# Optimization experiments

Hardware: AMD Instinct MI355X
Metric: run time of the kernel (lower is better)

The kernel has to match this reference:

```python
import jax, jax.numpy as jnp
import numpy as np

B, N, D, H = 64, 257, 1024, 16
HD = D // H  # 64


def setup_inputs() -> dict:
    key = jax.random.key(0)
    k1, k2, k3, k4, k5, k6 = jax.random.split(key, 6)
    x = jax.random.normal(k1, (B, N, D), dtype=jnp.float32)
    # boolean key mask per batch; never mask CLS token (col 0) so no fully-masked rows
    mask = jax.random.randint(k2, (B, N), 0, 2) > 0
    mask = mask.at[:, 0].set(False)
    s = 1.0 / np.sqrt(D)
    in_proj_w = jax.random.normal(k3, (3 * D, D), dtype=jnp.float32) * s
    in_proj_b = jax.random.normal(k4, (3 * D,), dtype=jnp.float32) * 0.02
    out_proj_w = jax.random.normal(k5, (D, D), dtype=jnp.float32) * s
    out_proj_b = jax.random.normal(k6, (D,), dtype=jnp.float32) * 0.02
    return {"x": x, "mask": mask, "in_proj_w": in_proj_w, "in_proj_b": in_proj_b,
            "out_proj_w": out_proj_w, "out_proj_b": out_proj_b}


def reference(x, mask, in_proj_w, in_proj_b, out_proj_w, out_proj_b):
    b, n, d = x.shape
    h, hd = H, d // H
    # fused QKV projection: [b, n, 3*d]
    qkv = jnp.einsum('bnd,ed->bne', x, in_proj_w) + in_proj_b
    # einops 'b n (qkv h d) -> qkv b h n d'
    qkv = qkv.reshape(b, n, 3, h, hd).transpose(2, 0, 3, 1, 4)
    q, k, v = qkv[0], qkv[1], qkv[2]  # each [b, h, n, hd]
    attn_weights = jnp.einsum('bhqe,bhke->bhqk', q, k) / jnp.sqrt(jnp.asarray(hd, x.dtype))
    # mode == 'mask': -inf on masked keys (broadcast over heads and queries)
    attn_weights = jnp.where(mask[:, None, None, :], -jnp.inf, attn_weights)
    attn_matrix = jax.nn.softmax(attn_weights, axis=-1)
    out = jnp.einsum('bhqk,bhke->bhqe', attn_matrix, v)  # [b, h, n, hd]
    out = out.transpose(0, 2, 1, 3).reshape(b, n, d)      # 'b h n d -> b n (h d)'
    return jnp.einsum('bnd,ed->bne', out, out_proj_w) + out_proj_b
```

## Files before the change

### kernel.cpp

```cpp
#include <hip/hip_runtime.h>

#define B_   64
#define N_   257
#define D_   1024
#define H_   16
#define HD_  64
#define M_   (B_*N_)
#define CK_  96
#define VTS_ 128
#define PLS_ 104

typedef __bf16 bf16x8 __attribute__((ext_vector_type(8)));
typedef __bf16 bf16x4 __attribute__((ext_vector_type(4)));
typedef float  f32x4  __attribute__((ext_vector_type(4)));

__device__ __forceinline__ void gload_lds16(const void* g, void* l) {
    __builtin_amdgcn_global_load_lds(
        (const __attribute__((address_space(1))) void*)g,
        (__attribute__((address_space(3))) void*)l, 16, 0, 0);
}

#define MEMF() asm volatile("" ::: "memory")
#define BARRIER() do { MEMF(); __builtin_amdgcn_s_barrier(); MEMF(); } while (0)
#define WAITV(n) asm volatile("s_waitcnt vmcnt(" #n ")" ::: "memory")

#define XQ_  4210688
#define W1Q_ 786432
#define W2Q_ 262144
__global__ __launch_bounds__(256) void cvt_all(const float* __restrict__ x,
                                               const float* __restrict__ w1,
                                               const float* __restrict__ w2,
                                               __bf16* __restrict__ xb,
                                               __bf16* __restrict__ w1b,
                                               __bf16* __restrict__ w2b) {
    int i = blockIdx.x * 256 + threadIdx.x;
    const float* src; __bf16* dst; int j;
    if (i < XQ_) { src = x; dst = xb; j = i; }
    else if (i < XQ_ + W1Q_) { src = w1; dst = w1b; j = i - XQ_; }
    else if (i < XQ_ + W1Q_ + W2Q_) { src = w2; dst = w2b; j = i - XQ_ - W1Q_; }
    else return;
    float4 v = reinterpret_cast<const float4*>(src)[j];
    bf16x4 o;
    o[0] = (__bf16)v.x; o[1] = (__bf16)v.y; o[2] = (__bf16)v.z; o[3] = (__bf16)v.w;
    *reinterpret_cast<bf16x4*>(dst + (size_t)j * 4) = o;
}

template<int NT, int MODE>
__global__ __launch_bounds__(512, 2) void gemm256(const __bf16* __restrict__ A,
                                                  const __bf16* __restrict__ W,
                                                  const float* __restrict__ bias,
                                                  __bf16* __restrict__ qo,
                                                  __bf16* __restrict__ ko,
                                                  __bf16* __restrict__ vo,
                                                  float* __restrict__ fo) {
    __shared__ __align__(16) char smem[131072];
    constexpr int NWG = 64 * NT;
    constexpr int qd = NWG >> 3;
    const int orig = blockIdx.x;
    const int xcd = orig & 7, loc = orig >> 3;
    const int wgid = xcd * qd + loc;
    const int rowt = wgid / NT, colt = wgid - rowt * NT;
    const int row0 = rowt * 256, col0 = colt * 256;

    const int tid = threadIdx.x, lane = tid & 63, wv = tid >> 6;
    const int wm = wv >> 2, wn = wv & 3;
    const int fr = lane & 15, fq = lane >> 4, frs = lane & 7;

    const int pr = tid >> 3;
    const int pg = ((tid & 7) ^ (pr & 7)) * 8;
    int srcA[4];
    {
        const int prow[4] = {0, 128, 64, 192};
#pragma unroll
        for (int p = 0; p < 4; ++p) {
            const int rg = row0 + prow[p] + pr;
            srcA[p] = rg * 1024 + pg;
        }
    }
    int srcW[2], ldsW[2];
#pragma unroll
    for (int e = 0; e < 2; ++e) {
        const int wb = (wv >> 1) * 64 + e * 16 + (wv & 1) * 8;
        srcW[e] = (col0 + wb + (lane >> 3)) * 1024 + pg;
        ldsW[e] = wb * 128;
    }
    char* const At0 = smem;
    char* const At1 = smem + 32768;
    char* const Wt0 = smem + 65536;
    char* const Wt1 = smem + 98304;

#define STG_AF(dst, kk) do { gload_lds16(A + srcA[0] + (kk), (dst) + wv * 1024); \
                             gload_lds16(A + srcA[1] + (kk), (dst) + 16384 + wv * 1024); } while (0)
#define STG_AB(dst, kk) do { gload_lds16(A + srcA[2] + (kk), (dst) + 8192 + wv * 1024); \
                             gload_lds16(A + srcA[3] + (kk), (dst) + 24576 + wv * 1024); } while (0)
#define STG_WF(dst, kk) do { gload_lds16(W + srcW[0] + (kk), (dst) + ldsW[0]); \
                             gload_lds16(W + srcW[1] + (kk), (dst) + ldsW[1]); } while (0)
#define STG_WB(dst, kk) do { gload_lds16(W + srcW[0] + 32768 + (kk), (dst) + ldsW[0] + 4096); \
                             gload_lds16(W + srcW[1] + 32768 + (kk), (dst) + ldsW[1] + 4096); } while (0)
#define LD_A(buf, rqo) do { \
    _Pragma("unroll") for (int i = 0; i < 4; ++i) \
    _Pragma("unroll") for (int ks = 0; ks < 2; ++ks) \
        af[i][ks] = *(const bf16x8*)((buf) + (wm * 128 + (rqo) + i * 16 + fr) * 128 \
                                           + (((ks * 4 + fq) ^ frs) << 4)); \
} while (0)
#define LD_B(buf, co, bw) do { \
    _Pragma("unroll") for (int j = 0; j < 2; ++j) \
    _Pragma("unroll") for (int ks = 0; ks < 2; ++ks) \
        bw[j][ks] = *(const bf16x8*)((buf) + (wn * 64 + (co) + j * 16 + fr) * 128 \
                                           + (((ks * 4 + fq) ^ frs) << 4)); \
} while (0)
#define MFMA_Q(i0, j0, bw) do { \
    __builtin_amdgcn_s_setprio(1); \
    _Pragma("unroll") for (int i = 0; i < 4; ++i) \
    _Pragma("unroll") for (int j = 0; j < 2; ++j) \
    _Pragma("unroll") for (int ks = 0; ks < 2; ++ks) \
        acc[(i0) + i][(j0) + j] = __builtin_amdgcn_mfma_f32_16x16x32_bf16( \
            af[i][ks], bw[j][ks], acc[(i0) + i][(j0) + j], 0, 0, 0); \
    __builtin_amdgcn_s_setprio(0); \
} while (0)

    f32x4 acc[8][4] = {};
    bf16x8 af[4][2], bw0[2][2], bw1[2][2];

    STG_AF(At0, 0); STG_WF(Wt0, 0); STG_WB(Wt0, 0); STG_AB(At0, 0);
    WAITV(0);
    BARRIER();

#pragma unroll 2
    for (int t = 0; t < 16; ++t) {
        char* const Ac = (t & 1) ? At1 : At0;
        char* const Wc = (t & 1) ? Wt1 : Wt0;
        char* const An = (t & 1) ? At0 : At1;
        char* const Wn = (t & 1) ? Wt0 : Wt1;
        if (t < 15) {
            const int kk = (t + 1) * 64;
            STG_AF(An, kk); STG_WF(Wn, kk); STG_WB(Wn, kk); STG_AB(An, kk);
        }
        LD_A(Ac, 0);
        LD_B(Wc, 0, bw0);
        LD_B(Wc, 32, bw1);
        MFMA_Q(0, 0, bw0);
        MFMA_Q(0, 2, bw1);
        LD_A(Ac, 64);
        MFMA_Q(4, 2, bw1);
        MFMA_Q(4, 0, bw0);
        WAITV(0);
        BARRIER();
    }

    if constexpr (MODE == 0) {
        const int which = colt >> 2;
        __bf16* const dst = which == 0 ? qo : (which == 1 ? ko : vo);
        const float scale = which == 0 ? 0.125f : 1.0f;
        float bj[4];
#pragma unroll
        for (int j = 0; j < 4; ++j) bj[j] = bias[col0 + wn * 64 + j * 16 + fr];
        __bf16* const Ct = (__bf16*)smem;
#pragma unroll
        for (int i = 0; i < 8; ++i) {
            const int rb = wm * 128 + (i >> 2) * 64 + (i & 3) * 16 + fq * 4;
#pragma unroll
            for (int r = 0; r < 4; ++r) {
                const int row = rb + r;
#pragma unroll
                for (int j = 0; j < 4; ++j) {
                    const int cu = wn * 64 + j * 16 + fr;
                    Ct[row * 256 + (((cu >> 3) ^ (row & 7)) * 8) + (cu & 7)] =
                        (__bf16)((acc[i][j][r] + bj[j]) * scale);
                }
            }
        }
        BARRIER();
#pragma unroll
        for (int p = 0; p < 16; ++p) {
            const int row = p * 16 + (tid >> 5);
            const int m = row0 + row;
            const int gl = tid & 31;
            bf16x8 v = *(const bf16x8*)(Ct + row * 256 + ((gl ^ (row & 7)) * 8));
            const int cG = col0 + gl * 8;
            const int h = (cG >> 6) & 15, hd = cG & 63;
            const int bb = m / 257, nn = m - bb * 257;
            *reinterpret_cast<bf16x8*>(dst + ((size_t)(bb * 16 + h) * 257 + nn) * 64 + hd) = v;
        }
    } else {
        float bj[4];
#pragma unroll
        for (int j = 0; j < 4; ++j) bj[j] = bias[col0 + wn * 64 + j * 16 + fr];
#pragma unroll
        for (int i = 0; i < 8; ++i) {
            const int rb = wm * 128 + (i >> 2) * 64 + (i & 3) * 16 + fq * 4;
#pragma unroll
            for (int r = 0; r < 4; ++r) {
                const int m = row0 + rb + r;
                float* const p = fo + (size_t)m * 1024 + col0 + wn * 64 + fr;
#pragma unroll
                for (int j = 0; j < 4; ++j) p[j * 16] = acc[i][j][r] + bj[j];
            }
        }
    }
#undef STG_AF
#undef STG_AB
#undef STG_WF
#undef STG_WB
#undef LD_A
#undef LD_B
#undef MFMA_Q
}

template<int MODE>
__global__ __launch_bounds__(256) void gemm_tail(const __bf16* __restrict__ A,
                                                 const __bf16* __restrict__ W,
                                                 const float* __restrict__ bias,
                                                 __bf16* __restrict__ qo,
                                                 __bf16* __restrict__ ko,
                                                 __bf16* __restrict__ vo,
                                                 float* __restrict__ fo) {
    __shared__ __align__(16) __bf16 As[64 * 64];
    __shared__ __align__(16) __bf16 Ws[128 * 64];
    const int col0 = blockIdx.x * 128;
    const int tid = threadIdx.x, lane = tid & 63, wv = tid >> 6;
    const int fr = lane & 15, fq = lane >> 4, frs = lane & 7;

    f32x4 acc[4][2] = {};
    for (int k0 = 0; k0 < 1024; k0 += 64) {
        __syncthreads();
#pragma unroll
        for (int i = 0; i < 2; ++i) {
            const int c = tid + i * 256;
            const int r = c >> 3, g = (c & 7) ^ (r & 7);
            gload_lds16(A + (size_t)(16384 + r) * 1024 + g * 8 + k0,
                        (char*)As + i * 4096 + wv * 1024);
        }
#pragma unroll
        for (int i = 0; i < 4; ++i) {
            const int c = tid + i * 256;
            const int r = c >> 3, g = (c & 7) ^ (r & 7);
            gload_lds16(W + (size_t)(col0 + r) * 1024 + g * 8 + k0,
                        (char*)Ws + i * 4096 + wv * 1024);
        }
        __syncthreads();
#pragma unroll
        for (int ks = 0; ks < 2; ++ks) {
            const int goff = ((ks * 4 + fq) ^ frs) * 8;
            bf16x8 af[4], bw[2];
#pragma unroll
            for (int i = 0; i < 4; ++i)
                af[i] = *reinterpret_cast<const bf16x8*>(&As[(i * 16 + fr) * 64 + goff]);
#pragma unroll
            for (int j = 0; j < 2; ++j)
                bw[j] = *reinterpret_cast<const bf16x8*>(&Ws[(wv * 32 + j * 16 + fr) * 64 + goff]);
#pragma unroll
            for (int i = 0; i < 4; ++i)
#pragma unroll
                for (int j = 0; j < 2; ++j)
                    acc[i][j] = __builtin_amdgcn_mfma_f32_16x16x32_bf16(af[i], bw[j], acc[i][j], 0, 0, 0);
        }
    }
#pragma unroll
    for (int i = 0; i < 4; ++i)
#pragma unroll
        for (int r = 0; r < 4; ++r) {
            const int rowC = i * 16 + fq * 4 + r;
            const int nn = 193 + rowC;
#pragma unroll
            for (int j = 0; j < 2; ++j) {
                const int cG = col0 + wv * 32 + j * 16 + fr;
                if constexpr (MODE == 0) {
                    const int which = cG >> 10;
                    __bf16* const dst = which == 0 ? qo : (which == 1 ? ko : vo);
                    const float scale = which == 0 ? 0.125f : 1.0f;
                    const int h = (cG >> 6) & 15, hd = cG & 63;
                    dst[((size_t)(63 * 16 + h) * 257 + nn) * 64 + hd] =
                        (__bf16)((acc[i][j][r] + bias[cG]) * scale);
                } else {
                    fo[(size_t)(16384 + rowC) * 1024 + cG] = acc[i][j][r] + bias[cG];
                }
            }
        }
}

__global__ __launch_bounds__(256) void attn_kernel(const __bf16* __restrict__ qw,
                                                   const __bf16* __restrict__ kw,
                                                   const __bf16* __restrict__ vw,
                                                   const int* __restrict__ mask,
                                                   __bf16* __restrict__ attn) {
    const int l = blockIdx.x;
    const int x = l & 7, rr = l >> 3;
    const int bh = x * 128 + (rr >> 2);
    const int q0 = (rr & 3) * 64;
    const int bb = bh >> 4, hh = bh & 15;
    const int tid = threadIdx.x, lane = tid & 63, wv = tid >> 6;
    const int fr = lane & 15, fq = lane >> 4;
    const float NEG_INF = -__builtin_inff();

    __shared__ __align__(16) __bf16 Qs[64 * 64];
    __shared__ __align__(16) __bf16 Ks[CK_ * 64];
    __shared__ __align__(16) __bf16 Vt[64 * VTS_];
    __shared__ __align__(16) __bf16 Pl[4][16 * PLS_];
    __shared__ float maskb[288];

    const __bf16* qg = qw + ((size_t)bh * 257 + q0) * 64;
    const __bf16* kg = kw + (size_t)bh * 257 * 64;
    const __bf16* vg = vw + (size_t)bh * 257 * 64;
    const int* mg = mask + bb * 257;

    for (int idx = tid; idx < 288; idx += 256)
        maskb[idx] = (idx < 257 && mg[idx] == 0) ? 0.0f : NEG_INF;

#pragma unroll
    for (int i = 0; i < 2; ++i) {
        const int c = tid + i * 256;
        const int r = c >> 3, g = (c & 7) ^ (r & 7);
        gload_lds16(qg + (size_t)r * 64 + g * 8, (char*)Qs + i * 4096 + wv * 1024);
    }

    float m_run[4] = {NEG_INF, NEG_INF, NEG_INF, NEG_INF};
    float l_run[4] = {};
    f32x4 Oa[4] = {};

    for (int c3 = 0; c3 < 3; ++c3) {
        const int k0 = c3 * CK_;
        __syncthreads();
#pragma unroll
        for (int i = 0; i < 3; ++i) {
            const int c = tid + i * 256;
            const int r = c >> 3, g = (c & 7) ^ (r & 7);
            if (k0 + r < 257)
                gload_lds16(kg + (size_t)(k0 + r) * 64 + g * 8, (char*)Ks + i * 4096 + wv * 1024);
        }
#pragma unroll
        for (int it = 0; it < 3; ++it) {
            const int t = tid + it * 256;
            const int key = t >> 3, grp = t & 7;
            if (k0 + key < 257) {
                bf16x8 v8 = *reinterpret_cast<const bf16x8*>(vg + (size_t)(k0 + key) * 64 + grp * 8);
#pragma unroll
                for (int u = 0; u < 8; ++u) {
                    const int hd = grp * 8 + u;
                    Vt[hd * VTS_ + (((key >> 3) ^ (hd & 7)) * 8) + (key & 7)] = v8[u];
                }
            }
        }
        __syncthreads();

        f32x4 s[6];
        {
            bf16x8 aq[2];
#pragma unroll
            for (int ks = 0; ks < 2; ++ks)
                aq[ks] = *reinterpret_cast<const bf16x8*>(
                    &Qs[(wv * 16 + fr) * 64 + (((ks * 4 + fq) ^ (fr & 7)) * 8)]);
#pragma unroll
            for (int nt = 0; nt < 6; ++nt) {
                f32x4 sa = {};
#pragma unroll
                for (int ks = 0; ks < 2; ++ks) {
                    bf16x8 bk = *reinterpret_cast<const bf16x8*>(
                        &Ks[(nt * 16 + fr) * 64 + (((ks * 4 + fq) ^ (fr & 7)) * 8)]);
                    sa = __builtin_amdgcn_mfma_f32_16x16x32_bf16(aq[ks], bk, sa, 0, 0, 0);
                }
                const float mb = maskb[k0 + nt * 16 + fr];
#pragma unroll
                for (int r = 0; r < 4; ++r) sa[r] += mb;
                s[nt] = sa;
            }
        }
        float alpha[4];
#pragma unroll
        for (int r = 0; r < 4; ++r) {
            float v = s[0][r];
#pragma unroll
            for (int nt = 1; nt < 6; ++nt) v = fmaxf(v, s[nt][r]);
            v = fmaxf(v, __shfl_xor(v, 1));
            v = fmaxf(v, __shfl_xor(v, 2));
            v = fmaxf(v, __shfl_xor(v, 4));
            v = fmaxf(v, __shfl_xor(v, 8));
            const float mnew = fmaxf(m_run[r], v);
            alpha[r] = __expf(m_run[r] - mnew);
            m_run[r] = mnew;
        }
        float sm[4] = {};
#pragma unroll
        for (int nt = 0; nt < 6; ++nt)
#pragma unroll
            for (int r = 0; r < 4; ++r) {
                const float p = __expf(s[nt][r] - m_run[r]);
                s[nt][r] = p;
                sm[r] += p;
            }
#pragma unroll
        for (int r = 0; r < 4; ++r) {
            float v = sm[r];
            v += __shfl_xor(v, 1);
            v += __shfl_xor(v, 2);
            v += __shfl_xor(v, 4);
            v += __shfl_xor(v, 8);
            l_run[r] = l_run[r] * alpha[r] + v;
        }
#pragma unroll
        for (int ot = 0; ot < 4; ++ot)
#pragma unroll
            for (int r = 0; r < 4; ++r) Oa[ot][r] *= alpha[r];
#pragma unroll
        for (int nt = 0; nt < 6; ++nt)
#pragma unroll
            for (int r = 0; r < 4; ++r)
                Pl[wv][(fq * 4 + r) * PLS_ + nt * 16 + fr] = (__bf16)s[nt][r];
        __syncthreads();
        bf16x8 ap[3];
#pragma unroll
        for (int kk = 0; kk < 3; ++kk)
            ap[kk] = *reinterpret_cast<const bf16x8*>(&Pl[wv][fr * PLS_ + kk * 32 + fq * 8]);
#pragma unroll
        for (int ot = 0; ot < 4; ++ot) {
            const int row = ot * 16 + fr;
#pragma unroll
            for (int kk = 0; kk < 3; ++kk) {
                bf16x8 bv = *reinterpret_cast<const bf16x8*>(
                    &Vt[row * VTS_ + (((kk * 4 + fq) ^ (fr & 7)) * 8)]);
                Oa[ot] = __builtin_amdgcn_mfma_f32_16x16x32_bf16(ap[kk], bv, Oa[ot], 0, 0, 0);
            }
        }
    }
#pragma unroll
    for (int r = 0; r < 4; ++r) {
        const int n = q0 + wv * 16 + fq * 4 + r;
        const float inv = 1.0f / l_run[r];
#pragma unroll
        for (int ot = 0; ot < 4; ++ot)
            attn[((size_t)(bb * 257 + n)) * 1024 + hh * 64 + ot * 16 + fr] =
                (__bf16)(Oa[ot][r] * inv);
    }
}

__global__ __launch_bounds__(320) void attn_tail(const __bf16* __restrict__ qw,
                                                 const __bf16* __restrict__ kw,
                                                 const __bf16* __restrict__ vw,
                                                 const int* __restrict__ mask,
                                                 __bf16* __restrict__ attn) {
    const int bh = blockIdx.x;
    const int bb = bh >> 4, hh = bh & 15;
    const int tid = threadIdx.x, wv = tid >> 6;
    const float NEG_INF = -__builtin_inff();
    __shared__ float pbuf[257];
    __shared__ float red[5];
    __shared__ float gstat[2];

    const __bf16* qg = qw + ((size_t)bh * 257 + 256) * 64;
    const __bf16* kg = kw + (size_t)bh * 257 * 64;
    const __bf16* vg = vw + (size_t)bh * 257 * 64;

    float s = NEG_INF;
    if (tid < 257) {
        const __bf16* kr = kg + (size_t)tid * 64;
        float acc = 0.0f;
#pragma unroll
        for (int g = 0; g < 8; ++g) {
            bf16x8 qv = *reinterpret_cast<const bf16x8*>(qg + g * 8);
            bf16x8 kv = *reinterpret_cast<const bf16x8*>(kr + g * 8);
#pragma unroll
            for (int u = 0; u < 8; ++u) acc += (float)qv[u] * (float)kv[u];
        }
        s = (mask[bb * 257 + tid] == 0) ? acc : NEG_INF;
    }
    float v = s;
#pragma unroll
    for (int d = 1; d < 64; d <<= 1) v = fmaxf(v, __shfl_xor(v, d));
    if ((tid & 63) == 0) red[wv] = v;
    __syncthreads();
    if (tid == 0) {
        float m = red[0];
#pragma unroll
        for (int w = 1; w < 5; ++w) m = fmaxf(m, red[w]);
        gstat[0] = m;
    }
    __syncthreads();
    const float gmax = gstat[0];
    float p = (tid < 257) ? __expf(s - gmax) : 0.0f;
    if (tid < 257) pbuf[tid] = p;
    float sv = p;
#pragma unroll
    for (int d = 1; d < 64; d <<= 1) sv += __shfl_xor(sv, d);
    if ((tid & 63) == 0) red[wv] = sv;
    __syncthreads();
    if (tid == 0) gstat[1] = red[0] + red[1] + red[2] + red[3] + red[4];
    __syncthreads();
    if (tid < 64) {
        const float inv = 1.0f / gstat[1];
        float o = 0.0f;
        for (int j = 0; j < 257; ++j)
            o += pbuf[j] * (float)vg[(size_t)j * 64 + tid];
        attn[((size_t)(bb * 257 + 256)) * 1024 + hh * 64 + tid] = (__bf16)(o * inv);
    }
}

extern "C" void kernel_launch(void* const* d_in, const int* in_sizes, int n_in,
                              void* d_out, int out_size, void* d_ws, size_t ws_size,
                              hipStream_t stream) {
    const float* x  = (const float*)d_in[0];
    const int* mask = (const int*)d_in[1];
    const float* w1 = (const float*)d_in[2];
    const float* b1 = (const float*)d_in[3];
    const float* w2 = (const float*)d_in[4];
    const float* b2 = (const float*)d_in[5];
    float* out = (float*)d_out;
    char* ws = (char*)d_ws;
    __bf16* x_bf  = (__bf16*)(ws);
    __bf16* w1_bf = (__bf16*)(ws + 33816576);
    __bf16* w2_bf = (__bf16*)(ws + 40108032);
    __bf16* q_ws  = (__bf16*)(ws + 42205184);
    __bf16* k_ws  = (__bf16*)(ws + 75890688);
    __bf16* v_ws  = (__bf16*)(ws + 109576192);
    __bf16* a_bf  = (__bf16*)(ws + 143261696);

    cvt_all<<<20544, 256, 0, stream>>>(x, w1, w2, x_bf, w1_bf, w2_bf);
    gemm256<12, 0><<<768, 512, 0, stream>>>(x_bf, w1_bf, b1, q_ws, k_ws, v_ws, nullptr);
    gemm_tail<0><<<24, 256, 0, stream>>>(x_bf, w1_bf, b1, q_ws, k_ws, v_ws, nullptr);
    attn_kernel<<<4096, 256, 0, stream>>>(q_ws, k_ws, v_ws, mask, a_bf);
    attn_tail<<<1024, 320, 0, stream>>>(q_ws, k_ws, v_ws, mask, a_bf);
    gemm256<4, 1><<<256, 512, 0, stream>>>(a_bf, w2_bf, b2, nullptr, nullptr, nullptr, out);
    gemm_tail<1><<<8, 256, 0, stream>>>(a_bf, w2_bf, b2, nullptr, nullptr, nullptr, out);
}
```

Before: 411.2 us.

## Merge tail kernels into main launches and prefetch K/V in attention

The separate tail GEMM and tail attention kernels are folded into the main kernels as extra workgroups at the end of the grid, which cuts the launch count from seven to four and lets the tail work run alongside the main tiles. The attention kernel now prefetches the next K chunk into LDS and the next V chunk into registers during the current chunk's compute. It uses explicit waitcnt and barriers in place of full syncthreads. Tail workgroups now use 512- or 256-thread configurations, and the extra registers for the V prefetch could lower occupancy.

After: 418.3 us. About the same (+1.7%).

```diff
diff --git a/kernel.cpp b/kernel.cpp
--- a/kernel.cpp
+++ b/kernel.cpp
@@ -23,6 +23,7 @@
 #define MEMF() asm volatile("" ::: "memory")
 #define BARRIER() do { MEMF(); __builtin_amdgcn_s_barrier(); MEMF(); } while (0)
 #define WAITV(n) asm volatile("s_waitcnt vmcnt(" #n ")" ::: "memory")
+#define WAITL(n) asm volatile("s_waitcnt lgkmcnt(" #n ")" ::: "memory")
 
 #define XQ_  4210688
 #define W1Q_ 786432
@@ -55,16 +56,69 @@
                                                   float* __restrict__ fo) {
     __shared__ __align__(16) char smem[131072];
     constexpr int NWG = 64 * NT;
+    const int orig = blockIdx.x;
+    const int tid = threadIdx.x, lane = tid & 63, wv = tid >> 6;
+    const int fr = lane & 15, fq = lane >> 4, frs = lane & 7;
+
+    if (orig >= NWG) {
+        const int col0 = (orig - NWG) * 128;
+        __bf16* const As = (__bf16*)smem;
+        __bf16* const Ws = (__bf16*)(smem + 8192);
+        f32x4 acc[4] = {};
+        for (int k0 = 0; k0 < 1024; k0 += 64) {
+            __syncthreads();
+            {
+                const int r = tid >> 3, g = (tid & 7) ^ (r & 7);
+                gload_lds16(A + (size_t)(16384 + r) * 1024 + g * 8 + k0,
+                            (char*)As + wv * 1024);
+            }
+#pragma unroll
+            for (int i = 0; i < 2; ++i) {
+                const int c = tid + i * 512;
+                const int r = c >> 3, g = (c & 7) ^ (r & 7);
+                gload_lds16(W + (size_t)(col0 + r) * 1024 + g * 8 + k0,
+                            (char*)Ws + i * 8192 + wv * 1024);
+            }
+            __syncthreads();
+#pragma unroll
+            for (int ks = 0; ks < 2; ++ks) {
+                const int goff = ((ks * 4 + fq) ^ frs) * 8;
+                bf16x8 a4[4], bw;
+#pragma unroll
+                for (int i = 0; i < 4; ++i)
+                    a4[i] = *reinterpret_cast<const bf16x8*>(&As[(i * 16 + fr) * 64 + goff]);
+                bw = *reinterpret_cast<const bf16x8*>(&Ws[(wv * 16 + fr) * 64 + goff]);
+#pragma unroll
+                for (int i = 0; i < 4; ++i)
+                    acc[i] = __builtin_amdgcn_mfma_f32_16x16x32_bf16(a4[i], bw, acc[i], 0, 0, 0);
+            }
+        }
+#pragma unroll
+        for (int i = 0; i < 4; ++i)
+#pragma unroll
+            for (int r = 0; r < 4; ++r) {
+                const int rowC = i * 16 + fq * 4 + r;
+                const int cG = col0 + wv * 16 + fr;
+                if constexpr (MODE == 0) {
+                    const int which = cG >> 10;
+                    __bf16* const dst = which == 0 ? qo : (which == 1 ? ko : vo);
+                    const float scale = which == 0 ? 0.125f : 1.0f;
+                    const int h = (cG >> 6) & 15, hd = cG & 63;
+                    dst[((size_t)(63 * 16 + h) * 257 + (193 + rowC)) * 64 + hd] =
+                        (__bf16)((acc[i][r] + bias[cG]) * scale);
+                } else {
+                    fo[(size_t)(16384 + rowC) * 1024 + cG] = acc[i][r] + bias[cG];
+                }
+            }
+        return;
+    }
+
     constexpr int qd = NWG >> 3;
-    const int orig = blockIdx.x;
     const int xcd = orig & 7, loc = orig >> 3;
     const int wgid = xcd * qd + loc;
     const int rowt = wgid / NT, colt = wgid - rowt * NT;
     const int row0 = rowt * 256, col0 = colt * 256;
-
-    const int tid = threadIdx.x, lane = tid & 63, wv = tid >> 6;
     const int wm = wv >> 2, wn = wv & 3;
-    const int fr = lane & 15, fq = lane >> 4, frs = lane & 7;
 
     const int pr = tid >> 3;
     const int pg = ((tid & 7) ^ (pr & 7)) * 8;
@@ -207,90 +261,13 @@
 #undef MFMA_Q
 }
 
-template<int MODE>
-__global__ __launch_bounds__(256) void gemm_tail(const __bf16* __restrict__ A,
-                                                 const __bf16* __restrict__ W,
-                                                 const float* __restrict__ bias,
-                                                 __bf16* __restrict__ qo,
-                                                 __bf16* __restrict__ ko,
-                                                 __bf16* __restrict__ vo,
-                                                 float* __restrict__ fo) {
-    __shared__ __align__(16) __bf16 As[64 * 64];
-    __shared__ __align__(16) __bf16 Ws[128 * 64];
-    const int col0 = blockIdx.x * 128;
+__global__ __launch_bounds__(256) void attn_all(const __bf16* __restrict__ qw,
+                                                const __bf16* __restrict__ kw,
+                                                const __bf16* __restrict__ vw,
+                                                const int* __restrict__ mask,
+                                                __bf16* __restrict__ attn) {
+    const int l = blockIdx.x;
     const int tid = threadIdx.x, lane = tid & 63, wv = tid >> 6;
-    const int fr = lane & 15, fq = lane >> 4, frs = lane & 7;
-
-    f32x4 acc[4][2] = {};
-    for (int k0 = 0; k0 < 1024; k0 += 64) {
-        __syncthreads();
-#pragma unroll
-        for (int i = 0; i < 2; ++i) {
-            const int c = tid + i * 256;
-            const int r = c >> 3, g = (c & 7) ^ (r & 7);
-            gload_lds16(A + (size_t)(16384 + r) * 1024 + g * 8 + k0,
-                        (char*)As + i * 4096 + wv * 1024);
-        }
-#pragma unroll
-        for (int i = 0; i < 4; ++i) {
-            const int c = tid + i * 256;
-            const int r = c >> 3, g = (c & 7) ^ (r & 7);
-            gload_lds16(W + (size_t)(col0 + r) * 1024 + g * 8 + k0,
-                        (char*)Ws + i * 4096 + wv * 1024);
-        }
-        __syncthreads();
-#pragma unroll
-        for (int ks = 0; ks < 2; ++ks) {
-            const int goff = ((ks * 4 + fq) ^ frs) * 8;
-            bf16x8 af[4], bw[2];
-#pragma unroll
-            for (int i = 0; i < 4; ++i)
-                af[i] = *reinterpret_cast<const bf16x8*>(&As[(i * 16 + fr) * 64 + goff]);
-#pragma unroll
-            for (int j = 0; j < 2; ++j)
-                bw[j] = *reinterpret_cast<const bf16x8*>(&Ws[(wv * 32 + j * 16 + fr) * 64 + goff]);
-#pragma unroll
-            for (int i = 0; i < 4; ++i)
-#pragma unroll
-                for (int j = 0; j < 2; ++j)
-                    acc[i][j] = __builtin_amdgcn_mfma_f32_16x16x32_bf16(af[i], bw[j], acc[i][j], 0, 0, 0);
-        }
-    }
-#pragma unroll
-    for (int i = 0; i < 4; ++i)
-#pragma unroll
-        for (int r = 0; r < 4; ++r) {
-            const int rowC = i * 16 + fq * 4 + r;
-            const int nn = 193 + rowC;
-#pragma unroll
-            for (int j = 0; j < 2; ++j) {
-                const int cG = col0 + wv * 32 + j * 16 + fr;
-                if constexpr (MODE == 0) {
-                    const int which = cG >> 10;
-                    __bf16* const dst = which == 0 ? qo : (which == 1 ? ko : vo);
-                    const float scale = which == 0 ? 0.125f : 1.0f;
-                    const int h = (cG >> 6) & 15, hd = cG & 63;
-                    dst[((size_t)(63 * 16 + h) * 257 + nn) * 64 + hd] =
-                        (__bf16)((acc[i][j][r] + bias[cG]) * scale);
-                } else {
-                    fo[(size_t)(16384 + rowC) * 1024 + cG] = acc[i][j][r] + bias[cG];
-                }
-            }
-        }
-}
-
-__global__ __launch_bounds__(256) void attn_kernel(const __bf16* __restrict__ qw,
-                                                   const __bf16* __restrict__ kw,
-                                                   const __bf16* __restrict__ vw,
-                                                   const int* __restrict__ mask,
-                                                   __bf16* __restrict__ attn) {
-    const int l = blockIdx.x;
-    const int x = l & 7, rr = l >> 3;
-    const int bh = x * 128 + (rr >> 2);
-    const int q0 = (rr & 3) * 64;
-    const int bb = bh >> 4, hh = bh & 15;
-    const int tid = threadIdx.x, lane = tid & 63, wv = tid >> 6;
-    const int fr = lane & 15, fq = lane >> 4;
     const float NEG_INF = -__builtin_inff();
 
     __shared__ __align__(16) __bf16 Qs[64 * 64];
@@ -298,21 +275,103 @@
     __shared__ __align__(16) __bf16 Vt[64 * VTS_];
     __shared__ __align__(16) __bf16 Pl[4][16 * PLS_];
     __shared__ float maskb[288];
+    __shared__ float pbufT[257];
+    __shared__ float redT[4];
+    __shared__ float gstatT[2];
+
+    if (l >= 4096) {
+        const int bh = l - 4096;
+        const int bb = bh >> 4, hh = bh & 15;
+        const __bf16* qg = qw + ((size_t)bh * 257 + 256) * 64;
+        const __bf16* kg = kw + (size_t)bh * 257 * 64;
+        const __bf16* vg = vw + (size_t)bh * 257 * 64;
+        float acc = 0.0f;
+        {
+            const __bf16* kr = kg + (size_t)tid * 64;
+#pragma unroll
+            for (int g = 0; g < 8; ++g) {
+                bf16x8 qv = *reinterpret_cast<const bf16x8*>(qg + g * 8);
+                bf16x8 kv = *reinterpret_cast<const bf16x8*>(kr + g * 8);
+#pragma unroll
+                for (int u = 0; u < 8; ++u) acc += (float)qv[u] * (float)kv[u];
+            }
+        }
+        float s0 = (mask[bb * 257 + tid] == 0) ? acc : NEG_INF;
+        float s1 = NEG_INF;
+        if (tid == 0) {
+            const __bf16* kr = kg + (size_t)256 * 64;
+            float a2 = 0.0f;
+#pragma unroll
+            for (int g = 0; g < 8; ++g) {
+                bf16x8 qv = *reinterpret_cast<const bf16x8*>(qg + g * 8);
+                bf16x8 kv = *reinterpret_cast<const bf16x8*>(kr + g * 8);
+#pragma unroll
+                for (int u = 0; u < 8; ++u) a2 += (float)qv[u] * (float)kv[u];
+            }
+            s1 = (mask[bb * 257 + 256] == 0) ? a2 : NEG_INF;
+        }
+        float v = fmaxf(s0, s1);
+#pragma unroll
+        for (int d = 1; d < 64; d <<= 1) v = fmaxf(v, __shfl_xor(v, d));
+        if (lane == 0) redT[wv] = v;
+        __syncthreads();
+        if (tid == 0) gstatT[0] = fmaxf(fmaxf(redT[0], redT[1]), fmaxf(redT[2], redT[3]));
+        __syncthreads();
+        const float gmax = gstatT[0];
+        float p0 = __expf(s0 - gmax);
+        pbufT[tid] = p0;
+        float sv = p0;
+        if (tid == 0) { const float p1 = __expf(s1 - gmax); pbufT[256] = p1; sv += p1; }
+#pragma unroll
+        for (int d = 1; d < 64; d <<= 1) sv += __shfl_xor(sv, d);
+        if (lane == 0) redT[wv] = sv;
+        __syncthreads();
+        if (tid == 0) gstatT[1] = redT[0] + redT[1] + redT[2] + redT[3];
+        __syncthreads();
+        if (tid < 64) {
+            const float inv = 1.0f / gstatT[1];
+            float o = 0.0f;
+            for (int j = 0; j < 257; ++j)
+                o += pbufT[j] * (float)vg[(size_t)j * 64 + tid];
+            attn[((size_t)(bb * 257 + 256)) * 1024 + hh * 64 + tid] = (__bf16)(o * inv);
+        }
+        return;
+    }
+
+    const int x = l & 7, rr = l >> 3;
+    const int bh = x * 128 + (rr >> 2);
+    const int q0 = (rr & 3) * 64;
+    const int bb = bh >> 4, hh = bh & 15;
+    const int fr = lane & 15, fq = lane >> 4;
 
     const __bf16* qg = qw + ((size_t)bh * 257 + q0) * 64;
     const __bf16* kg = kw + (size_t)bh * 257 * 64;
     const __bf16* vg = vw + (size_t)bh * 257 * 64;
     const int* mg = mask + bb * 257;
 
+#define STG_K(k0v) do { _Pragma("unroll") for (int i = 0; i < 3; ++i) { \
+        const int c = tid + i * 256; const int r = c >> 3; \
+        int rg = (k0v) + r; if (rg > 256) rg = 256; \
+        const int g = (c & 7) ^ (r & 7); \
+        gload_lds16(kg + (size_t)rg * 64 + g * 8, (char*)Ks + i * 4096 + wv * 1024); } } while (0)
+#define LDV(k0v) do { _Pragma("unroll") for (int it = 0; it < 3; ++it) { \
+        const int t = tid + it * 256; int key = (k0v) + (t >> 3); \
+        if (key > 256) key = 256; \
+        vreg[it] = *reinterpret_cast<const bf16x8*>(vg + (size_t)key * 64 + (t & 7) * 8); } } while (0)
+
     for (int idx = tid; idx < 288; idx += 256)
         maskb[idx] = (idx < 257 && mg[idx] == 0) ? 0.0f : NEG_INF;
 
+    bf16x8 vreg[3];
 #pragma unroll
     for (int i = 0; i < 2; ++i) {
         const int c = tid + i * 256;
         const int r = c >> 3, g = (c & 7) ^ (r & 7);
         gload_lds16(qg + (size_t)r * 64 + g * 8, (char*)Qs + i * 4096 + wv * 1024);
     }
+    STG_K(0);
+    MEMF();
+    LDV(0);
 
     float m_run[4] = {NEG_INF, NEG_INF, NEG_INF, NEG_INF};
     float l_run[4] = {};
@@ -320,28 +379,9 @@
 
     for (int c3 = 0; c3 < 3; ++c3) {
         const int k0 = c3 * CK_;
-        __syncthreads();
-#pragma unroll
-        for (int i = 0; i < 3; ++i) {
-            const int c = tid + i * 256;
-            const int r = c >> 3, g = (c & 7) ^ (r & 7);
-            if (k0 + r < 257)
-                gload_lds16(kg + (size_t)(k0 + r) * 64 + g * 8, (char*)Ks + i * 4096 + wv * 1024);
-        }
-#pragma unroll
-        for (int it = 0; it < 3; ++it) {
-            const int t = tid + it * 256;
-            const int key = t >> 3, grp = t & 7;
-            if (k0 + key < 257) {
-                bf16x8 v8 = *reinterpret_cast<const bf16x8*>(vg + (size_t)(k0 + key) * 64 + grp * 8);
-#pragma unroll
-                for (int u = 0; u < 8; ++u) {
-                    const int hd = grp * 8 + u;
-                    Vt[hd * VTS_ + (((key >> 3) ^ (hd & 7)) * 8) + (key & 7)] = v8[u];
-                }
-            }
-        }
-        __syncthreads();
+        WAITL(0);
+        WAITV(3);
+        BARRIER();
 
         f32x4 s[6];
         {
@@ -363,6 +403,17 @@
 #pragma unroll
                 for (int r = 0; r < 4; ++r) sa[r] += mb;
                 s[nt] = sa;
+            }
+        }
+        WAITV(0);
+#pragma unroll
+        for (int it = 0; it < 3; ++it) {
+            const int t = tid + it * 256;
+            const int key = t >> 3, grp = t & 7;
+#pragma unroll
+            for (int u = 0; u < 8; ++u) {
+                const int hd = grp * 8 + u;
+                Vt[hd * VTS_ + (((key >> 3) ^ (hd & 7)) * 8) + (key & 7)] = vreg[it][u];
             }
         }
         float alpha[4];
@@ -406,7 +457,13 @@
 #pragma unroll
             for (int r = 0; r < 4; ++r)
                 Pl[wv][(fq * 4 + r) * PLS_ + nt * 16 + fr] = (__bf16)s[nt][r];
-        __syncthreads();
+        WAITL(0);
+        BARRIER();
+        if (c3 < 2) {
+            STG_K(k0 + CK_);
+            MEMF();
+            LDV(k0 + CK_);
+        }
         bf16x8 ap[3];
 #pragma unroll
         for (int kk = 0; kk < 3; ++kk)
@@ -431,67 +488,8 @@
             attn[((size_t)(bb * 257 + n)) * 1024 + hh * 64 + ot * 16 + fr] =
                 (__bf16)(Oa[ot][r] * inv);
     }
-}
-
-__global__ __launch_bounds__(320) void attn_tail(const __bf16* __restrict__ qw,
-                                                 const __bf16* __restrict__ kw,
-                                                 const __bf16* __restrict__ vw,
-                                                 const int* __restrict__ mask,
-                                                 __bf16* __restrict__ attn) {
-    const int bh = blockIdx.x;
-    const int bb = bh >> 4, hh = bh & 15;
-    const int tid = threadIdx.x, wv = tid >> 6;
-    const float NEG_INF = -__builtin_inff();
-    __shared__ float pbuf[257];
-    __shared__ float red[5];
-    __shared__ float gstat[2];
-
-    const __bf16* qg = qw + ((size_t)bh * 257 + 256) * 64;
-    const __bf16* kg = kw + (size_t)bh * 257 * 64;
-    const __bf16* vg = vw + (size_t)bh * 257 * 64;
-
-    float s = NEG_INF;
-    if (tid < 257) {
-        const __bf16* kr = kg + (size_t)tid * 64;
-        float acc = 0.0f;
-#pragma unroll
-        for (int g = 0; g < 8; ++g) {
-            bf16x8 qv = *reinterpret_cast<const bf16x8*>(qg + g * 8);
-            bf16x8 kv = *reinterpret_cast<const bf16x8*>(kr + g * 8);
-#pragma unroll
-            for (int u = 0; u < 8; ++u) acc += (float)qv[u] * (float)kv[u];
-        }
-        s = (mask[bb * 257 + tid] == 0) ? acc : NEG_INF;
-    }
-    float v = s;
-#pragma unroll
-    for (int d = 1; d < 64; d <<= 1) v = fmaxf(v, __shfl_xor(v, d));
-    if ((tid & 63) == 0) red[wv] = v;
-    __syncthreads();
-    if (tid == 0) {
-        float m = red[0];
-#pragma unroll
-        for (int w = 1; w < 5; ++w) m = fmaxf(m, red[w]);
-        gstat[0] = m;
-    }
-    __syncthreads();
-    const float gmax = gstat[0];
-    float p = (tid < 257) ? __expf(s - gmax) : 0.0f;
-    if (tid < 257) pbuf[tid] = p;
-    float sv = p;
-#pragma unroll
-    for (int d = 1; d < 64; d <<= 1) sv += __shfl_xor(sv, d);
-    if ((tid & 63) == 0) red[wv] = sv;
-    __syncthreads();
-    if (tid == 0) gstat[1] = red[0] + red[1] + red[2] + red[3] + red[4];
-    __syncthreads();
-    if (tid < 64) {
-        const float inv = 1.0f / gstat[1];
-        float o = 0.0f;
-        for (int j = 0; j < 257; ++j)
-            o += pbuf[j] * (float)vg[(size_t)j * 64 + tid];
-        attn[((size_t)(bb * 257 + 256)) * 1024 + hh * 64 + tid] = (__bf16)(o * inv);
-    }
+#undef STG_K
+#undef LDV
 }
 
 extern "C" void kernel_launch(void* const* d_in, const int* in_sizes, int n_in,
@@ -514,10 +512,7 @@
     __bf16* a_bf  = (__bf16*)(ws + 143261696);
 
     cvt_all<<<20544, 256, 0, stream>>>(x, w1, w2, x_bf, w1_bf, w2_bf);
-    gemm256<12, 0><<<768, 512, 0, stream>>>(x_bf, w1_bf, b1, q_ws, k_ws, v_ws, nullptr);
-    gemm_tail<0><<<24, 256, 0, stream>>>(x_bf, w1_bf, b1, q_ws, k_ws, v_ws, nullptr);
-    attn_kernel<<<4096, 256, 0, stream>>>(q_ws, k_ws, v_ws, mask, a_bf);
-    attn_tail<<<1024, 320, 0, stream>>>(q_ws, k_ws, v_ws, mask, a_bf);
-    gemm256<4, 1><<<256, 512, 0, stream>>>(a_bf, w2_bf, b2, nullptr, nullptr, nullptr, out);
-    gemm_tail<1><<<8, 256, 0, stream>>>(a_bf, w2_bf, b2, nullptr, nullptr, nullptr, out);
+    gemm256<12, 0><<<792, 512, 0, stream>>>(x_bf, w1_bf, b1, q_ws, k_ws, v_ws, nullptr);
+    attn_all<<<5120, 256, 0, stream>>>(q_ws, k_ws, v_ws, mask, a_bf);
+    gemm256<4, 1><<<264, 512, 0, stream>>>(a_bf, w2_bf, b2, nullptr, nullptr, nullptr, out);
 }
```
